# Kernel tuning notes

Hardware: AMD Instinct MI355X
Metric: run time of the kernel (lower is better)

Reference implementation:

```python
import jax, jax.numpy as jnp
import numpy as np

EMBED_DIM = 1024


def setup_inputs() -> dict:
    key = jax.random.key(0)
    ks = jax.random.split(key, 9)
    d = EMBED_DIM
    s = 1.0 / np.sqrt(d)
    x = jax.random.normal(ks[0], (4, 2048, d), dtype=jnp.float32)
    # nn.Linear weights are [out, in]; we store them transposed for x @ W
    Wq = jax.random.uniform(ks[1], (d, d), jnp.float32, -s, s)
    bq = jax.random.uniform(ks[2], (d,), jnp.float32, -s, s)
    Wk = jax.random.uniform(ks[3], (d, d), jnp.float32, -s, s)
    bk = jax.random.uniform(ks[4], (d,), jnp.float32, -s, s)
    Wv = jax.random.uniform(ks[5], (d, d), jnp.float32, -s, s)
    bv = jax.random.uniform(ks[6], (d,), jnp.float32, -s, s)
    Wo = jax.random.uniform(ks[7], (d, d), jnp.float32, -s, s)
    bo = jax.random.uniform(ks[8], (d,), jnp.float32, -s, s)
    return {"x": x, "Wq": Wq, "bq": bq, "Wk": Wk, "bk": bk,
            "Wv": Wv, "bv": bv, "Wo": Wo, "bo": bo}


def reference(x, Wq, bq, Wk, bk, Wv, bv, Wo, bo):
    b, seq_len, d = x.shape
    scaling = 1.0 / jnp.sqrt(jnp.float32(d))
    q = x @ Wq + bq  # [b, s, d]
    k = x @ Wk + bk
    v = x @ Wv + bv
    scores = jnp.einsum('bqd,bkd->bqk', q, k) * scaling  # [b, s, s]
    causal = jnp.tril(jnp.ones((seq_len, seq_len), dtype=bool))
    scores = jnp.where(causal, scores, -jnp.inf)
    attn = jax.nn.softmax(scores, axis=-1)
    out = jnp.einsum('bqk,bkd->bqd', attn, v)
    return out @ Wo + bo
```

## Files before the change

kernel.cpp:

```cpp
#include <hip/hip_runtime.h>
#include <stdint.h>

typedef __bf16 bf16_t;
typedef __bf16 bf16x8 __attribute__((ext_vector_type(8)));
typedef __bf16 bf16x4 __attribute__((ext_vector_type(4)));
typedef float  f32x4  __attribute__((ext_vector_type(4)));

#define DEV __device__ __forceinline__

constexpr int S = 2048, D = 1024, BATCH = 4, MF = BATCH * S;

DEV void gload16(const void* g, void* l) {
  __builtin_amdgcn_global_load_lds(
      (const __attribute__((address_space(1))) void*)g,
      (__attribute__((address_space(3))) void*)(uint32_t)(uintptr_t)l,
      16, 0, 0);
}

template<int EP>
DEV void gemm_body(int tm, int tn, int bz,
                   const bf16_t* __restrict__ A, const bf16_t* __restrict__ B,
                   void* __restrict__ C0, void* __restrict__ C1,
                   void* __restrict__ C2, const float* __restrict__ aux,
                   int K, int kmax, bf16_t* ldsA, bf16_t* ldsB)
{
  const int m0 = tm * 128, n0 = tn * 128;
  const int tid  = threadIdx.x;
  const int lane = tid & 63;
  const int wave = tid >> 6;
  const int wm = wave & 1, wn = wave >> 1;
  const int l8r = lane >> 3;
  const int swz = ((lane & 7) ^ (lane >> 3)) * 8;
  const int cl  = lane & 15;
  const int qd  = lane >> 4;
  const int ch0 = ((qd ^ (cl & 7)) * 8);

  f32x4 acc[4][4] = {};

  for (int k0 = 0; k0 < kmax; k0 += 64) {
    #pragma unroll
    for (int t = 0; t < 4; ++t) {
      const int rb = wave * 4 + t;
      gload16(A + (long)(m0 + rb * 8 + l8r) * K + (k0 + swz), &ldsA[rb * 512]);
      gload16(B + (long)(n0 + rb * 8 + l8r) * K + (k0 + swz), &ldsB[rb * 512]);
    }
    __syncthreads();
    #pragma unroll
    for (int kk = 0; kk < 64; kk += 32) {
      bf16x8 af[4], bg[4];
      #pragma unroll
      for (int i = 0; i < 4; ++i)
        af[i] = *(const bf16x8*)&ldsA[(wm * 64 + i * 16 + cl) * 64 + (ch0 ^ kk)];
      #pragma unroll
      for (int j = 0; j < 4; ++j)
        bg[j] = *(const bf16x8*)&ldsB[(wn * 64 + j * 16 + cl) * 64 + (ch0 ^ kk)];
      #pragma unroll
      for (int i = 0; i < 4; ++i)
        #pragma unroll
        for (int j = 0; j < 4; ++j)
          acc[i][j] = __builtin_amdgcn_mfma_f32_16x16x32_bf16(af[i], bg[j], acc[i][j], 0, 0, 0);
    }
    __syncthreads();
  }

  #pragma unroll
  for (int i = 0; i < 4; ++i) {
    const int gm0 = m0 + wm * 64 + i * 16 + qd * 4;

    if (EP == 1) {
      uint8_t* q8 = (uint8_t*)C0;
      uint8_t* k8 = (uint8_t*)C1;
      bf16_t* vwT = (bf16_t*)C2;
      #pragma unroll
      for (int j = 0; j < 4; ++j) {
        const int gn  = n0 + wn * 64 + j * 16 + cl;
        const int sec = gn >> 10, ln = gn & 1023;
        const float bn = aux[gn];
        if (sec == 2) {
          const int z = gm0 >> 11, s0 = gm0 & 2047;
          bf16x4 v4;
          #pragma unroll
          for (int r = 0; r < 4; ++r) v4[r] = (bf16_t)(acc[i][j][r] + bn);
          *(bf16x4*)&vwT[((long)z * D + ln) * S + s0] = v4;
        } else {
          uint8_t* dst = (sec == 0) ? q8 : k8;
          #pragma unroll
          for (int r = 0; r < 4; ++r) {
            const float v = acc[i][j][r] + bn;
            const int p = __builtin_amdgcn_cvt_pk_fp8_f32(v, v, 0, false);
            dst[(long)(gm0 + r) * D + ln] = (uint8_t)(p & 0xFF);
          }
        }
      }
    }

    if (EP == 3) {
      float* out = (float*)C0 + (long)bz * S * D;
      const float* invl = aux + (long)bz * S;
      const float* bo = (const float*)C1;
      float scl[4];
      #pragma unroll
      for (int r = 0; r < 4; ++r) scl[r] = invl[gm0 + r];
      #pragma unroll
      for (int j = 0; j < 4; ++j) {
        const int gn = n0 + wn * 64 + j * 16 + cl;
        const float bn = bo[gn];
        #pragma unroll
        for (int r = 0; r < 4; ++r)
          out[(long)(gm0 + r) * D + gn] = acc[i][j][r] * scl[r] + bn;
      }
    }

    if (EP == 4) {
      bf16_t* Co = (bf16_t*)C0;
      #pragma unroll
      for (int j = 0; j < 4; ++j) {
        const int gn = n0 + wn * 64 + j * 16 + cl;
        #pragma unroll
        for (int r = 0; r < 4; ++r)
          Co[(long)(gm0 + r) * D + gn] = (bf16_t)acc[i][j][r];
      }
    }
  }
}

__global__ __launch_bounds__(256, 4) void gemm_qkv(
    const bf16_t* __restrict__ A, const bf16_t* __restrict__ B,
    uint8_t* q8, uint8_t* k8, bf16_t* vwT, const float* __restrict__ bias)
{
  __shared__ __align__(16) bf16_t lA[128 * 64], lB[128 * 64];
  gemm_body<1>(blockIdx.x, blockIdx.y, 0, A, B, q8, k8, vwT, bias,
               1024, 1024, lA, lB);
}

__global__ __launch_bounds__(256, 4) void gemm_sc8(
    const uint8_t* __restrict__ q8g, const uint8_t* __restrict__ k8g,
    bf16_t* __restrict__ probs_g, float* __restrict__ part)
{
  __shared__ __align__(16) uint8_t lA[128 * 64], lB[128 * 64];
  const int l = blockIdx.x, xcd = l & 7, idx = l >> 3;
  const int bz = xcd >> 1;
  const int t  = (xcd & 1) * 68 + idx;
  int tm = (int)((sqrtf(8.0f * t + 1.0f) - 1.0f) * 0.5f);
  while ((tm + 1) * (tm + 2) / 2 <= t) ++tm;
  while (tm * (tm + 1) / 2 > t) --tm;
  const int tn = t - tm * (tm + 1) / 2;
  const int m0 = tm * 128, n0 = tn * 128;
  const uint8_t* q8 = q8g + (long)bz * S * D;
  const uint8_t* k8 = k8g + (long)bz * S * D;

  const int tid  = threadIdx.x;
  const int lane = tid & 63;
  const int wave = tid >> 6;
  const int wm = wave & 1, wn = wave >> 1;
  const int srow = lane >> 2;
  const int sgr  = (lane & 3) ^ ((lane >> 3) & 3);
  const int cl = lane & 15, qd = lane >> 4;
  const int sfr = (cl >> 1) & 3;
  const int half8 = (qd & 1) * 8;

  f32x4 acc[4][4] = {};

  for (int k0 = 0; k0 < 1024; k0 += 64) {
    #pragma unroll
    for (int tt = 0; tt < 2; ++tt) {
      const int rb = wave * 2 + tt;
      const int gr = rb * 16 + srow;
      gload16(q8 + (long)(m0 + gr) * 1024 + k0 + sgr * 16, &lA[rb * 1024]);
      gload16(k8 + (long)(n0 + gr) * 1024 + k0 + sgr * 16, &lB[rb * 1024]);
    }
    __syncthreads();
    #pragma unroll
    for (int kk = 0; kk < 2; ++kk) {
      long a[4], b[4];
      const int pg = ((kk << 1) + (qd >> 1)) ^ sfr;
      #pragma unroll
      for (int i = 0; i < 4; ++i)
        a[i] = *(const long*)&lA[(wm * 64 + i * 16 + cl) * 64 + pg * 16 + half8];
      #pragma unroll
      for (int j = 0; j < 4; ++j)
        b[j] = *(const long*)&lB[(wn * 64 + j * 16 + cl) * 64 + pg * 16 + half8];
      #pragma unroll
      for (int i = 0; i < 4; ++i)
        #pragma unroll
        for (int j = 0; j < 4; ++j)
          acc[i][j] = __builtin_amdgcn_mfma_f32_16x16x32_fp8_fp8(a[i], b[j], acc[i][j], 0, 0, 0);
    }
    __syncthreads();
  }

  bf16_t* probs = probs_g + (long)bz * S * S;
  #pragma unroll
  for (int i = 0; i < 4; ++i) {
    const int gm0 = m0 + wm * 64 + i * 16 + qd * 4;
    float ls[4] = {0.f, 0.f, 0.f, 0.f};
    #pragma unroll
    for (int j = 0; j < 4; ++j) {
      const int gn = n0 + wn * 64 + j * 16 + cl;
      #pragma unroll
      for (int r = 0; r < 4; ++r) {
        const int gm = gm0 + r;
        const float e = (gn <= gm) ? __expf(acc[i][j][r] * 0.03125f) : 0.0f;
        probs[(long)gm * S + gn] = (bf16_t)e;
        ls[r] += e;
      }
    }
    #pragma unroll
    for (int r = 0; r < 4; ++r) {
      float v = ls[r];
      v += __shfl_xor(v, 1); v += __shfl_xor(v, 2);
      v += __shfl_xor(v, 4); v += __shfl_xor(v, 8);
      if (cl == 0)
        part[((long)bz * S + (gm0 + r)) * 32 + tn * 2 + wn] = v;
    }
  }
}

__global__ __launch_bounds__(256, 4) void gemm_pv_out(
    const bf16_t* __restrict__ probs, const bf16_t* __restrict__ vwT,
    float* out, const float* __restrict__ invl, const float* __restrict__ bo)
{
  __shared__ __align__(16) bf16_t lA[128 * 64], lB[128 * 64];
  const int l = blockIdx.x, xcd = l & 7, idx = l >> 3;
  const int bz = xcd >> 1, half = xcd & 1;
  const int g = (idx >> 3) & 3, tn = idx & 7;
  const int tm = (idx < 32) ? (15 - half - 2 * g) : (2 * g + half);
  const int kmax = (tm + 1) * 128;
  gemm_body<3>(tm, tn, bz, probs + (long)bz * S * S, vwT + (long)bz * D * S,
               out, (void*)bo, nullptr, invl, 2048, kmax, lA, lB);
}

__global__ __launch_bounds__(256, 4) void gemm_wvo(
    const bf16_t* __restrict__ WoT, const bf16_t* __restrict__ WvN,
    bf16_t* WvoT)
{
  __shared__ __align__(16) bf16_t lA[128 * 64], lB[128 * 64];
  gemm_body<4>(blockIdx.x, blockIdx.y, 0, WoT, WvN, WvoT, nullptr, nullptr,
               nullptr, 1024, 1024, lA, lB);
}

__global__ __launch_bounds__(256) void reduce_invl(
    const float* __restrict__ part, float* __restrict__ invl)
{
  const int r = blockIdx.x * 256 + threadIdx.x;
  const int row = r & (S - 1);
  const int cnt = ((row >> 7) + 1) * 2;
  const float* p = part + (long)r * 32;
  float s = 0.f;
  for (int j = 0; j < cnt; ++j) s += p[j];
  invl[r] = 1.0f / s;
}

__global__ __launch_bounds__(256) void cvt_x(
    const float4* __restrict__ in, bf16x4* __restrict__ out, int n4)
{
  const int i = blockIdx.x * 256 + threadIdx.x;
  if (i >= n4) return;
  float4 f = in[i];
  bf16x4 o;
  o.x = (__bf16)f.x; o.y = (__bf16)f.y; o.z = (__bf16)f.z; o.w = (__bf16)f.w;
  out[i] = o;
}

__global__ __launch_bounds__(256) void cvt_w_t4(
    const float* __restrict__ W0, const float* __restrict__ W1,
    const float* __restrict__ W2, const float* __restrict__ W3,
    bf16_t* __restrict__ dst)
{
  const int zmap[4] = {0, 1, 3, 4};
  const float* W = (blockIdx.z == 0) ? W0 : (blockIdx.z == 1) ? W1
                 : (blockIdx.z == 2) ? W2 : W3;
  bf16_t* WT = dst + (size_t)zmap[blockIdx.z] * D * D;
  const int bx = blockIdx.x, by = blockIdx.y;
  const int tx = threadIdx.x & 31, ty = threadIdx.x >> 5;

  if (blockIdx.z == 2) {
    #pragma unroll
    for (int dy = 0; dy < 32; dy += 8) {
      const long idx = (long)(by * 32 + ty + dy) * 1024 + bx * 32 + tx;
      WT[idx] = (bf16_t)W[idx];
    }
    return;
  }

  __shared__ float t[32][33];
  #pragma unroll
  for (int dy = 0; dy < 32; dy += 8)
    t[ty + dy][tx] = W[(long)(by * 32 + ty + dy) * 1024 + bx * 32 + tx];
  __syncthreads();
  #pragma unroll
  for (int dy = 0; dy < 32; dy += 8)
    WT[(long)(bx * 32 + ty + dy) * 1024 + by * 32 + tx] = (bf16_t)t[tx][ty + dy];
}

__global__ __launch_bounds__(256) void bias_build(
    const float* __restrict__ bq, const float* __restrict__ bk,
    const float* __restrict__ bv, const bf16_t* __restrict__ WoT,
    float* __restrict__ o)
{
  const int b = blockIdx.x;
  if (b >= 256) {
    const int i = (b - 256) * 256 + threadIdx.x;
    o[i] = bq[i];
    o[1024 + i] = bk[i];
    return;
  }
  const int wave = threadIdx.x >> 6, lane = threadIdx.x & 63;
  const int c = b * 4 + wave;
  const bf16_t* row = WoT + (long)c * 1024 + lane * 16;
  const float*  bvp = bv + lane * 16;
  float s = 0.f;
  #pragma unroll
  for (int j = 0; j < 16; ++j) s += bvp[j] * (float)row[j];
  #pragma unroll
  for (int sh = 32; sh > 0; sh >>= 1) s += __shfl_xor(s, sh, 64);
  if (lane == 0) o[2048 + c] = s;
}

extern "C" void kernel_launch(void* const* d_in, const int* in_sizes, int n_in,
                              void* d_out, int out_size, void* d_ws, size_t ws_size,
                              hipStream_t stream) {
  const float* x  = (const float*)d_in[0];
  const float* Wq = (const float*)d_in[1];
  const float* bq = (const float*)d_in[2];
  const float* Wk = (const float*)d_in[3];
  const float* bk = (const float*)d_in[4];
  const float* Wv = (const float*)d_in[5];
  const float* bv = (const float*)d_in[6];
  const float* Wo = (const float*)d_in[7];
  const float* bo = (const float*)d_in[8];
  float* out = (float*)d_out;

  size_t off = 0;
  auto alloc = [&](size_t bytes) -> void* {
    void* p = (char*)d_ws + off;
    off += (bytes + 255) & ~(size_t)255;
    return p;
  };
  bf16_t* x_b   = (bf16_t*)alloc((size_t)MF * D * 2);
  bf16_t* Wall  = (bf16_t*)alloc((size_t)5 * D * D * 2);
  float*  bqkv  = (float*) alloc((size_t)3 * D * 4);
  uint8_t* q8   = (uint8_t*)alloc((size_t)MF * D);
  uint8_t* k8   = (uint8_t*)alloc((size_t)MF * D);
  bf16_t* vwT_b = (bf16_t*)alloc((size_t)BATCH * D * S * 2);
  bf16_t* probs = (bf16_t*)alloc((size_t)BATCH * S * S * 2);
  float*  part  = (float*) alloc((size_t)MF * 32 * 4);
  float*  invl  = (float*) alloc((size_t)MF * 4);
  bf16_t* WqkvT = Wall;
  bf16_t* WvoT  = Wall + (size_t)2 * D * D;
  bf16_t* WvN   = Wall + (size_t)3 * D * D;
  bf16_t* WoT   = Wall + (size_t)4 * D * D;

  cvt_x<<<dim3((MF * D / 4 + 255) / 256), 256, 0, stream>>>(
      (const float4*)x, (bf16x4*)x_b, MF * D / 4);
  cvt_w_t4<<<dim3(32, 32, 4), 256, 0, stream>>>(Wq, Wk, Wv, Wo, Wall);
  bias_build<<<dim3(260), 256, 0, stream>>>(bq, bk, bv, WoT, bqkv);

  gemm_wvo<<<dim3(8, 8), 256, 0, stream>>>(WoT, WvN, WvoT);

  gemm_qkv<<<dim3(64, 24), 256, 0, stream>>>(x_b, WqkvT, q8, k8, vwT_b, bqkv);

  gemm_sc8<<<dim3(544), 256, 0, stream>>>(q8, k8, probs, part);

  reduce_invl<<<dim3(MF / 256), 256, 0, stream>>>(part, invl);

  gemm_pv_out<<<dim3(512), 256, 0, stream>>>(probs, vwT_b, out, invl, bo);
}
```

Before: 249.1 us.

## Replace QKV GEMM with 256x256-tile, 8-wave, double-buffered pipelined kernel

Replaces the 128x128-tile QKV projection GEMM with a dedicated 256x256-tile kernel using 512 threads, a double-buffered LDS pipeline of async global-to-LDS loads, and four interleaved MFMA quarter-phases separated by explicit barriers and setprio hints. Larger tiles raise arithmetic intensity and cut global traffic per FLOP. Overlapping the next K-slice loads with compute is meant to hide memory latency. In exchange it uses 128KB of LDS and many accumulator registers, which limits occupancy. The grid shrinks to 384 blocks, which may leave the 256 CUs unevenly loaded.

```diff
diff --git a/kernel.cpp b/kernel.cpp
--- a/kernel.cpp
+++ b/kernel.cpp
@@ -16,6 +16,9 @@
       (__attribute__((address_space(3))) void*)(uint32_t)(uintptr_t)l,
       16, 0, 0);
 }
+
+#define BAR() asm volatile("s_barrier" ::: "memory")
+#define WAIT_LGKM0() asm volatile("s_waitcnt lgkmcnt(0)" ::: "memory")
 
 template<int EP>
 DEV void gemm_body(int tm, int tn, int bz,
@@ -67,33 +70,6 @@
   for (int i = 0; i < 4; ++i) {
     const int gm0 = m0 + wm * 64 + i * 16 + qd * 4;
 
-    if (EP == 1) {
-      uint8_t* q8 = (uint8_t*)C0;
-      uint8_t* k8 = (uint8_t*)C1;
-      bf16_t* vwT = (bf16_t*)C2;
-      #pragma unroll
-      for (int j = 0; j < 4; ++j) {
-        const int gn  = n0 + wn * 64 + j * 16 + cl;
-        const int sec = gn >> 10, ln = gn & 1023;
-        const float bn = aux[gn];
-        if (sec == 2) {
-          const int z = gm0 >> 11, s0 = gm0 & 2047;
-          bf16x4 v4;
-          #pragma unroll
-          for (int r = 0; r < 4; ++r) v4[r] = (bf16_t)(acc[i][j][r] + bn);
-          *(bf16x4*)&vwT[((long)z * D + ln) * S + s0] = v4;
-        } else {
-          uint8_t* dst = (sec == 0) ? q8 : k8;
-          #pragma unroll
-          for (int r = 0; r < 4; ++r) {
-            const float v = acc[i][j][r] + bn;
-            const int p = __builtin_amdgcn_cvt_pk_fp8_f32(v, v, 0, false);
-            dst[(long)(gm0 + r) * D + ln] = (uint8_t)(p & 0xFF);
-          }
-        }
-      }
-    }
-
     if (EP == 3) {
       float* out = (float*)C0 + (long)bz * S * D;
       const float* invl = aux + (long)bz * S;
@@ -124,13 +100,153 @@
   }
 }
 
-__global__ __launch_bounds__(256, 4) void gemm_qkv(
+DEV void stA256(const bf16_t* A, int m0, int k0, bf16_t* dst,
+                int qh, int wave, int l8r, int swz) {
+  #pragma unroll
+  for (int t = 0; t < 2; ++t) {
+    const int ib = wave * 2 + t;
+    const int rb = ((ib >> 3) << 7) | (qh << 6) | ((ib & 7) << 3);
+    gload16(A + (long)(m0 + rb + l8r) * 1024 + (k0 + swz), dst + rb * 64);
+  }
+}
+
+DEV void stB256(const bf16_t* B, int n0, int k0, bf16_t* dst,
+                int qh, int wave, int l8r, int swz) {
+  #pragma unroll
+  for (int t = 0; t < 2; ++t) {
+    const int ib = wave * 2 + t;
+    const int rb = ((ib >> 2) << 6) | (qh << 5) | ((ib & 3) << 3);
+    gload16(B + (long)(n0 + rb + l8r) * 1024 + (k0 + swz), dst + rb * 64);
+  }
+}
+
+DEV void readA4(bf16x8 (&a)[4][2], const bf16_t* base, int row0, int cl, int ch0) {
+  #pragma unroll
+  for (int i = 0; i < 4; ++i) {
+    const bf16_t* p = base + (row0 + i * 16 + cl) * 64;
+    a[i][0] = *(const bf16x8*)(p + ch0);
+    a[i][1] = *(const bf16x8*)(p + (ch0 ^ 32));
+  }
+}
+
+DEV void readB2(bf16x8 (&b)[2][2], const bf16_t* base, int row0, int cl, int ch0) {
+  #pragma unroll
+  for (int jj = 0; jj < 2; ++jj) {
+    const bf16_t* p = base + (row0 + jj * 16 + cl) * 64;
+    b[jj][0] = *(const bf16x8*)(p + ch0);
+    b[jj][1] = *(const bf16x8*)(p + (ch0 ^ 32));
+  }
+}
+
+template<int MH, int NH>
+DEV void qphase(f32x4 (&acc)[8][4], const bf16x8 (&a)[4][2], const bf16x8 (&b)[2][2]) {
+  __builtin_amdgcn_s_setprio(1);
+  #pragma unroll
+  for (int i = 0; i < 4; ++i)
+    #pragma unroll
+    for (int jj = 0; jj < 2; ++jj)
+      #pragma unroll
+      for (int kk = 0; kk < 2; ++kk)
+        acc[MH * 4 + i][NH * 2 + jj] = __builtin_amdgcn_mfma_f32_16x16x32_bf16(
+            a[i][kk], b[jj][kk], acc[MH * 4 + i][NH * 2 + jj], 0, 0, 0);
+  __builtin_amdgcn_s_setprio(0);
+}
+
+__global__ __launch_bounds__(512, 2) void gemm_qkv256(
     const bf16_t* __restrict__ A, const bf16_t* __restrict__ B,
-    uint8_t* q8, uint8_t* k8, bf16_t* vwT, const float* __restrict__ bias)
-{
-  __shared__ __align__(16) bf16_t lA[128 * 64], lB[128 * 64];
-  gemm_body<1>(blockIdx.x, blockIdx.y, 0, A, B, q8, k8, vwT, bias,
-               1024, 1024, lA, lB);
+    uint8_t* __restrict__ q8, uint8_t* __restrict__ k8,
+    bf16_t* __restrict__ vwT, const float* __restrict__ aux)
+{
+  __shared__ __align__(16) bf16_t lA[2][256 * 64], lB[2][256 * 64];
+  const int m0 = blockIdx.x * 256, n0 = blockIdx.y * 256;
+  const int tid = threadIdx.x, lane = tid & 63, wave = tid >> 6;
+  const int wm = wave & 1, wn = wave >> 1;
+  const int l8r = lane >> 3, swz = ((lane & 7) ^ l8r) * 8;
+  const int cl = lane & 15, qd = lane >> 4;
+  const int ch0 = (qd ^ (cl & 7)) * 8;
+
+  f32x4 acc[8][4] = {};
+  bf16x8 a[4][2], b0[2][2], b1[2][2];
+
+  stA256(A, m0,  0, lA[0], 0, wave, l8r, swz);
+  stB256(B, n0,  0, lB[0], 0, wave, l8r, swz);
+  stB256(B, n0,  0, lB[0], 1, wave, l8r, swz);
+  stA256(A, m0,  0, lA[0], 1, wave, l8r, swz);
+  stA256(A, m0, 64, lA[1], 0, wave, l8r, swz);
+  stB256(B, n0, 64, lB[1], 0, wave, l8r, swz);
+  stB256(B, n0, 64, lB[1], 1, wave, l8r, swz);
+  asm volatile("s_waitcnt vmcnt(6)" ::: "memory");
+  BAR();
+
+  for (int t = 0; t < 16; ++t) {
+    const int cur = t & 1;
+    const bf16_t* cA = lA[cur];
+    const bf16_t* cB = lB[cur];
+    bf16_t* nAbuf = lA[cur ^ 1];
+    bf16_t* cAbuf = lA[cur];
+    bf16_t* cBbuf = lB[cur];
+    const int rA = wm * 128, rB = wn * 64;
+    const int kn1 = (t + 1) * 64, kn2 = (t + 2) * 64;
+
+    readA4(a, cA, rA, cl, ch0);
+    readB2(b0, cB, rB, cl, ch0);
+    if (t < 15) stA256(A, m0, kn1, nAbuf, 1, wave, l8r, swz);
+    BAR();
+    WAIT_LGKM0();
+    qphase<0, 0>(acc, a, b0);
+    BAR();
+
+    readB2(b1, cB, rB + 32, cl, ch0);
+    if (t < 14) stA256(A, m0, kn2, cAbuf, 0, wave, l8r, swz);
+    BAR();
+    WAIT_LGKM0();
+    qphase<0, 1>(acc, a, b1);
+    BAR();
+
+    readA4(a, cA, rA + 64, cl, ch0);
+    if (t < 14) stB256(B, n0, kn2, cBbuf, 0, wave, l8r, swz);
+    BAR();
+    WAIT_LGKM0();
+    qphase<1, 0>(acc, a, b0);
+    BAR();
+
+    if (t < 14) {
+      stB256(B, n0, kn2, cBbuf, 1, wave, l8r, swz);
+      asm volatile("s_waitcnt vmcnt(6)" ::: "memory");
+    } else if (t == 14) {
+      asm volatile("s_waitcnt vmcnt(0)" ::: "memory");
+    }
+    BAR();
+    WAIT_LGKM0();
+    qphase<1, 1>(acc, a, b1);
+    BAR();
+  }
+
+  #pragma unroll
+  for (int ai = 0; ai < 8; ++ai) {
+    const int gm0 = m0 + wm * 128 + ai * 16 + qd * 4;
+    #pragma unroll
+    for (int aj = 0; aj < 4; ++aj) {
+      const int gn  = n0 + wn * 64 + aj * 16 + cl;
+      const int sec = gn >> 10, ln = gn & 1023;
+      const float bn = aux[gn];
+      if (sec == 2) {
+        const int z = gm0 >> 11, s0 = gm0 & 2047;
+        bf16x4 v4;
+        #pragma unroll
+        for (int r = 0; r < 4; ++r) v4[r] = (bf16_t)(acc[ai][aj][r] + bn);
+        *(bf16x4*)&vwT[((long)z * D + ln) * S + s0] = v4;
+      } else {
+        uint8_t* dst = (sec == 0) ? q8 : k8;
+        #pragma unroll
+        for (int r = 0; r < 4; ++r) {
+          const float v = acc[ai][aj][r] + bn;
+          const int p = __builtin_amdgcn_cvt_pk_fp8_f32(v, v, 0, false);
+          dst[(long)(gm0 + r) * D + ln] = (uint8_t)(p & 0xFF);
+        }
+      }
+    }
+  }
 }
 
 __global__ __launch_bounds__(256, 4) void gemm_sc8(
@@ -358,7 +474,7 @@
 
   gemm_wvo<<<dim3(8, 8), 256, 0, stream>>>(WoT, WvN, WvoT);
 
-  gemm_qkv<<<dim3(64, 24), 256, 0, stream>>>(x_b, WqkvT, q8, k8, vwT_b, bqkv);
+  gemm_qkv256<<<dim3(32, 12), 512, 0, stream>>>(x_b, WqkvT, q8, k8, vwT_b, bqkv);
 
   gemm_sc8<<<dim3(544), 256, 0, stream>>>(q8, k8, probs, part);
 
```

Result: slower. 259.2 us (+4.1%).

## Use 64x128 score tiles and fold row-sum reduction into PV kernel

Applied to the files above, without the earlier changes.

The QK^T fp8 score kernel now uses 64-row by 128-column tiles, giving 1088 blocks over the causal triangle instead of 544 128x128 tiles. This trims wasted work on diagonal tiles and improves load balance, and the occupancy hint is raised to 6. The separate reduce_invl kernel is removed: the PV/output kernel now sums the per-row partial sums into shared memory before its GEMM, which saves a launch and an intermediate buffer. In exchange, the smaller tiles mean less data reuse per loaded byte, and every PV block redundantly re-reads the partials.

```diff
diff --git a/kernel.cpp b/kernel.cpp
--- a/kernel.cpp
+++ b/kernel.cpp
@@ -94,13 +94,13 @@
       }
     }
 
-    if (EP == 3) {
+    if (EP == 5) {
       float* out = (float*)C0 + (long)bz * S * D;
-      const float* invl = aux + (long)bz * S;
       const float* bo = (const float*)C1;
+      const float* invl_l = aux;
       float scl[4];
       #pragma unroll
-      for (int r = 0; r < 4; ++r) scl[r] = invl[gm0 + r];
+      for (int r = 0; r < 4; ++r) scl[r] = invl_l[wm * 64 + i * 16 + qd * 4 + r];
       #pragma unroll
       for (int j = 0; j < 4; ++j) {
         const int gn = n0 + wn * 64 + j * 16 + cl;
@@ -133,58 +133,60 @@
                1024, 1024, lA, lB);
 }
 
-__global__ __launch_bounds__(256, 4) void gemm_sc8(
+__global__ __launch_bounds__(256, 6) void gemm_sc8(
     const uint8_t* __restrict__ q8g, const uint8_t* __restrict__ k8g,
     bf16_t* __restrict__ probs_g, float* __restrict__ part)
 {
-  __shared__ __align__(16) uint8_t lA[128 * 64], lB[128 * 64];
+  __shared__ __align__(16) uint8_t lA[64 * 64], lB[128 * 64];
   const int l = blockIdx.x, xcd = l & 7, idx = l >> 3;
   const int bz = xcd >> 1;
-  const int t  = (xcd & 1) * 68 + idx;
-  int tm = (int)((sqrtf(8.0f * t + 1.0f) - 1.0f) * 0.5f);
-  while ((tm + 1) * (tm + 2) / 2 <= t) ++tm;
-  while (tm * (tm + 1) / 2 > t) --tm;
-  const int tn = t - tm * (tm + 1) / 2;
-  const int m0 = tm * 128, n0 = tn * 128;
+  const int t  = (xcd & 1) * 136 + idx;
+  int a0 = (int)((sqrtf(4.0f * t + 1.0f) - 1.0f) * 0.5f);
+  while ((a0 + 1) * (a0 + 2) <= t) ++a0;
+  while (a0 * (a0 + 1) > t) --a0;
+  int r64, tn;
+  if (t >= (a0 + 1) * (a0 + 1)) { r64 = 2 * a0 + 1; tn = t - (a0 + 1) * (a0 + 1); }
+  else                          { r64 = 2 * a0;     tn = t - a0 * (a0 + 1); }
+  const int m0 = r64 * 64, n0 = tn * 128;
   const uint8_t* q8 = q8g + (long)bz * S * D;
   const uint8_t* k8 = k8g + (long)bz * S * D;
 
   const int tid  = threadIdx.x;
   const int lane = tid & 63;
-  const int wave = tid >> 6;
-  const int wm = wave & 1, wn = wave >> 1;
+  const int wn   = tid >> 6;
   const int srow = lane >> 2;
   const int sgr  = (lane & 3) ^ ((lane >> 3) & 3);
   const int cl = lane & 15, qd = lane >> 4;
   const int sfr = (cl >> 1) & 3;
   const int half8 = (qd & 1) * 8;
 
-  f32x4 acc[4][4] = {};
+  f32x4 acc[4][2] = {};
 
   for (int k0 = 0; k0 < 1024; k0 += 64) {
+    gload16(q8 + (long)(m0 + wn * 16 + srow) * 1024 + k0 + sgr * 16,
+            &lA[wn * 1024]);
     #pragma unroll
     for (int tt = 0; tt < 2; ++tt) {
-      const int rb = wave * 2 + tt;
-      const int gr = rb * 16 + srow;
-      gload16(q8 + (long)(m0 + gr) * 1024 + k0 + sgr * 16, &lA[rb * 1024]);
-      gload16(k8 + (long)(n0 + gr) * 1024 + k0 + sgr * 16, &lB[rb * 1024]);
+      const int rb = wn * 2 + tt;
+      gload16(k8 + (long)(n0 + rb * 16 + srow) * 1024 + k0 + sgr * 16,
+              &lB[rb * 1024]);
     }
     __syncthreads();
     #pragma unroll
     for (int kk = 0; kk < 2; ++kk) {
-      long a[4], b[4];
+      long av[4], bv[2];
       const int pg = ((kk << 1) + (qd >> 1)) ^ sfr;
       #pragma unroll
       for (int i = 0; i < 4; ++i)
-        a[i] = *(const long*)&lA[(wm * 64 + i * 16 + cl) * 64 + pg * 16 + half8];
-      #pragma unroll
-      for (int j = 0; j < 4; ++j)
-        b[j] = *(const long*)&lB[(wn * 64 + j * 16 + cl) * 64 + pg * 16 + half8];
+        av[i] = *(const long*)&lA[(i * 16 + cl) * 64 + pg * 16 + half8];
+      #pragma unroll
+      for (int j = 0; j < 2; ++j)
+        bv[j] = *(const long*)&lB[(wn * 32 + j * 16 + cl) * 64 + pg * 16 + half8];
       #pragma unroll
       for (int i = 0; i < 4; ++i)
         #pragma unroll
-        for (int j = 0; j < 4; ++j)
-          acc[i][j] = __builtin_amdgcn_mfma_f32_16x16x32_fp8_fp8(a[i], b[j], acc[i][j], 0, 0, 0);
+        for (int j = 0; j < 2; ++j)
+          acc[i][j] = __builtin_amdgcn_mfma_f32_16x16x32_fp8_fp8(av[i], bv[j], acc[i][j], 0, 0, 0);
     }
     __syncthreads();
   }
@@ -192,11 +194,11 @@
   bf16_t* probs = probs_g + (long)bz * S * S;
   #pragma unroll
   for (int i = 0; i < 4; ++i) {
-    const int gm0 = m0 + wm * 64 + i * 16 + qd * 4;
+    const int gm0 = m0 + i * 16 + qd * 4;
     float ls[4] = {0.f, 0.f, 0.f, 0.f};
     #pragma unroll
-    for (int j = 0; j < 4; ++j) {
-      const int gn = n0 + wn * 64 + j * 16 + cl;
+    for (int j = 0; j < 2; ++j) {
+      const int gn = n0 + wn * 32 + j * 16 + cl;
       #pragma unroll
       for (int r = 0; r < 4; ++r) {
         const int gm = gm0 + r;
@@ -211,23 +213,35 @@
       v += __shfl_xor(v, 1); v += __shfl_xor(v, 2);
       v += __shfl_xor(v, 4); v += __shfl_xor(v, 8);
       if (cl == 0)
-        part[((long)bz * S + (gm0 + r)) * 32 + tn * 2 + wn] = v;
+        part[((long)bz * S + (gm0 + r)) * 64 + tn * 4 + wn] = v;
     }
   }
 }
 
 __global__ __launch_bounds__(256, 4) void gemm_pv_out(
     const bf16_t* __restrict__ probs, const bf16_t* __restrict__ vwT,
-    float* out, const float* __restrict__ invl, const float* __restrict__ bo)
+    float* out, const float* __restrict__ part, const float* __restrict__ bo)
 {
   __shared__ __align__(16) bf16_t lA[128 * 64], lB[128 * 64];
+  __shared__ float invl_s[128];
   const int l = blockIdx.x, xcd = l & 7, idx = l >> 3;
   const int bz = xcd >> 1, half = xcd & 1;
   const int g = (idx >> 3) & 3, tn = idx & 7;
   const int tm = (idx < 32) ? (15 - half - 2 * g) : (2 * g + half);
   const int kmax = (tm + 1) * 128;
-  gemm_body<3>(tm, tn, bz, probs + (long)bz * S * S, vwT + (long)bz * D * S,
-               out, (void*)bo, nullptr, invl, 2048, kmax, lA, lB);
+
+  if (threadIdx.x < 128) {
+    const int row = tm * 128 + threadIdx.x;
+    const int cnt = (tm + 1) * 4;
+    const float* p = part + ((long)bz * S + row) * 64;
+    float s = 0.f;
+    for (int j = 0; j < cnt; ++j) s += p[j];
+    invl_s[threadIdx.x] = 1.0f / s;
+  }
+  __syncthreads();
+
+  gemm_body<5>(tm, tn, bz, probs + (long)bz * S * S, vwT + (long)bz * D * S,
+               out, (void*)bo, nullptr, invl_s, 2048, kmax, lA, lB);
 }
 
 __global__ __launch_bounds__(256, 4) void gemm_wvo(
@@ -237,18 +251,6 @@
   __shared__ __align__(16) bf16_t lA[128 * 64], lB[128 * 64];
   gemm_body<4>(blockIdx.x, blockIdx.y, 0, WoT, WvN, WvoT, nullptr, nullptr,
                nullptr, 1024, 1024, lA, lB);
-}
-
-__global__ __launch_bounds__(256) void reduce_invl(
-    const float* __restrict__ part, float* __restrict__ invl)
-{
-  const int r = blockIdx.x * 256 + threadIdx.x;
-  const int row = r & (S - 1);
-  const int cnt = ((row >> 7) + 1) * 2;
-  const float* p = part + (long)r * 32;
-  float s = 0.f;
-  for (int j = 0; j < cnt; ++j) s += p[j];
-  invl[r] = 1.0f / s;
 }
 
 __global__ __launch_bounds__(256) void cvt_x(
@@ -344,8 +346,7 @@
   uint8_t* k8   = (uint8_t*)alloc((size_t)MF * D);
   bf16_t* vwT_b = (bf16_t*)alloc((size_t)BATCH * D * S * 2);
   bf16_t* probs = (bf16_t*)alloc((size_t)BATCH * S * S * 2);
-  float*  part  = (float*) alloc((size_t)MF * 32 * 4);
-  float*  invl  = (float*) alloc((size_t)MF * 4);
+  float*  part  = (float*) alloc((size_t)MF * 64 * 4);
   bf16_t* WqkvT = Wall;
   bf16_t* WvoT  = Wall + (size_t)2 * D * D;
   bf16_t* WvN   = Wall + (size_t)3 * D * D;
@@ -360,9 +361,7 @@
 
   gemm_qkv<<<dim3(64, 24), 256, 0, stream>>>(x_b, WqkvT, q8, k8, vwT_b, bqkv);
 
-  gemm_sc8<<<dim3(544), 256, 0, stream>>>(q8, k8, probs, part);
-
-  reduce_invl<<<dim3(MF / 256), 256, 0, stream>>>(part, invl);
-
-  gemm_pv_out<<<dim3(512), 256, 0, stream>>>(probs, vwT_b, out, invl, bo);
-}
+  gemm_sc8<<<dim3(1088), 256, 0, stream>>>(q8, k8, probs, part);
+
+  gemm_pv_out<<<dim3(512), 256, 0, stream>>>(probs, vwT_b, out, part, bo);
+}
```

New measurement: 250.6 us. Within noise of the previous version (+0.6%).

## Deepen K-step per barrier and fuse softmax row-sum reduction into PV GEMM

Applied to the files above, without the earlier changes.

The GEMM loops for the score and PV kernels now stage two 64-wide K slices per barrier pair, which halves synchronisation count per K and gives more loads in flight, at the cost of doubled LDS usage. The PV kernel's occupancy hint drops to 2. The separate reduce_invl kernel is removed and each PV block computes its 128 row inverse-sums from the partials into shared memory before the GEMM, saving a launch and a global round trip at the cost of redundant reduction across the 8 column tiles.

```diff
diff --git a/kernel.cpp b/kernel.cpp
--- a/kernel.cpp
+++ b/kernel.cpp
@@ -17,7 +17,7 @@
       16, 0, 0);
 }
 
-template<int EP>
+template<int EP, int NSUB>
 DEV void gemm_body(int tm, int tn, int bz,
                    const bf16_t* __restrict__ A, const bf16_t* __restrict__ B,
                    void* __restrict__ C0, void* __restrict__ C1,
@@ -37,28 +37,36 @@
 
   f32x4 acc[4][4] = {};
 
-  for (int k0 = 0; k0 < kmax; k0 += 64) {
-    #pragma unroll
-    for (int t = 0; t < 4; ++t) {
-      const int rb = wave * 4 + t;
-      gload16(A + (long)(m0 + rb * 8 + l8r) * K + (k0 + swz), &ldsA[rb * 512]);
-      gload16(B + (long)(n0 + rb * 8 + l8r) * K + (k0 + swz), &ldsB[rb * 512]);
+  for (int k0 = 0; k0 < kmax; k0 += 64 * NSUB) {
+    #pragma unroll
+    for (int h = 0; h < NSUB; ++h) {
+      #pragma unroll
+      for (int t = 0; t < 4; ++t) {
+        const int rb = wave * 4 + t;
+        gload16(A + (long)(m0 + rb * 8 + l8r) * K + (k0 + h * 64 + swz),
+                &ldsA[h * 8192 + rb * 512]);
+        gload16(B + (long)(n0 + rb * 8 + l8r) * K + (k0 + h * 64 + swz),
+                &ldsB[h * 8192 + rb * 512]);
+      }
     }
     __syncthreads();
     #pragma unroll
-    for (int kk = 0; kk < 64; kk += 32) {
-      bf16x8 af[4], bg[4];
-      #pragma unroll
-      for (int i = 0; i < 4; ++i)
-        af[i] = *(const bf16x8*)&ldsA[(wm * 64 + i * 16 + cl) * 64 + (ch0 ^ kk)];
-      #pragma unroll
-      for (int j = 0; j < 4; ++j)
-        bg[j] = *(const bf16x8*)&ldsB[(wn * 64 + j * 16 + cl) * 64 + (ch0 ^ kk)];
-      #pragma unroll
-      for (int i = 0; i < 4; ++i)
+    for (int h = 0; h < NSUB; ++h) {
+      #pragma unroll
+      for (int kk = 0; kk < 64; kk += 32) {
+        bf16x8 af[4], bg[4];
+        #pragma unroll
+        for (int i = 0; i < 4; ++i)
+          af[i] = *(const bf16x8*)&ldsA[h * 8192 + (wm * 64 + i * 16 + cl) * 64 + (ch0 ^ kk)];
         #pragma unroll
         for (int j = 0; j < 4; ++j)
-          acc[i][j] = __builtin_amdgcn_mfma_f32_16x16x32_bf16(af[i], bg[j], acc[i][j], 0, 0, 0);
+          bg[j] = *(const bf16x8*)&ldsB[h * 8192 + (wn * 64 + j * 16 + cl) * 64 + (ch0 ^ kk)];
+        #pragma unroll
+        for (int i = 0; i < 4; ++i)
+          #pragma unroll
+          for (int j = 0; j < 4; ++j)
+            acc[i][j] = __builtin_amdgcn_mfma_f32_16x16x32_bf16(af[i], bg[j], acc[i][j], 0, 0, 0);
+      }
     }
     __syncthreads();
   }
@@ -94,13 +102,13 @@
       }
     }
 
-    if (EP == 3) {
+    if (EP == 5) {
       float* out = (float*)C0 + (long)bz * S * D;
-      const float* invl = aux + (long)bz * S;
       const float* bo = (const float*)C1;
+      const float* invl_l = aux;
       float scl[4];
       #pragma unroll
-      for (int r = 0; r < 4; ++r) scl[r] = invl[gm0 + r];
+      for (int r = 0; r < 4; ++r) scl[r] = invl_l[wm * 64 + i * 16 + qd * 4 + r];
       #pragma unroll
       for (int j = 0; j < 4; ++j) {
         const int gn = n0 + wn * 64 + j * 16 + cl;
@@ -129,15 +137,15 @@
     uint8_t* q8, uint8_t* k8, bf16_t* vwT, const float* __restrict__ bias)
 {
   __shared__ __align__(16) bf16_t lA[128 * 64], lB[128 * 64];
-  gemm_body<1>(blockIdx.x, blockIdx.y, 0, A, B, q8, k8, vwT, bias,
-               1024, 1024, lA, lB);
+  gemm_body<1, 1>(blockIdx.x, blockIdx.y, 0, A, B, q8, k8, vwT, bias,
+                  1024, 1024, lA, lB);
 }
 
 __global__ __launch_bounds__(256, 4) void gemm_sc8(
     const uint8_t* __restrict__ q8g, const uint8_t* __restrict__ k8g,
     bf16_t* __restrict__ probs_g, float* __restrict__ part)
 {
-  __shared__ __align__(16) uint8_t lA[128 * 64], lB[128 * 64];
+  __shared__ __align__(16) uint8_t lA[2][128 * 64], lB[2][128 * 64];
   const int l = blockIdx.x, xcd = l & 7, idx = l >> 3;
   const int bz = xcd >> 1;
   const int t  = (xcd & 1) * 68 + idx;
@@ -161,30 +169,38 @@
 
   f32x4 acc[4][4] = {};
 
-  for (int k0 = 0; k0 < 1024; k0 += 64) {
-    #pragma unroll
-    for (int tt = 0; tt < 2; ++tt) {
-      const int rb = wave * 2 + tt;
-      const int gr = rb * 16 + srow;
-      gload16(q8 + (long)(m0 + gr) * 1024 + k0 + sgr * 16, &lA[rb * 1024]);
-      gload16(k8 + (long)(n0 + gr) * 1024 + k0 + sgr * 16, &lB[rb * 1024]);
+  for (int k0 = 0; k0 < 1024; k0 += 128) {
+    #pragma unroll
+    for (int h = 0; h < 2; ++h) {
+      #pragma unroll
+      for (int tt = 0; tt < 2; ++tt) {
+        const int rb = wave * 2 + tt;
+        const int gr = rb * 16 + srow;
+        gload16(q8 + (long)(m0 + gr) * 1024 + k0 + h * 64 + sgr * 16,
+                &lA[h][rb * 1024]);
+        gload16(k8 + (long)(n0 + gr) * 1024 + k0 + h * 64 + sgr * 16,
+                &lB[h][rb * 1024]);
+      }
     }
     __syncthreads();
     #pragma unroll
-    for (int kk = 0; kk < 2; ++kk) {
-      long a[4], b[4];
-      const int pg = ((kk << 1) + (qd >> 1)) ^ sfr;
-      #pragma unroll
-      for (int i = 0; i < 4; ++i)
-        a[i] = *(const long*)&lA[(wm * 64 + i * 16 + cl) * 64 + pg * 16 + half8];
-      #pragma unroll
-      for (int j = 0; j < 4; ++j)
-        b[j] = *(const long*)&lB[(wn * 64 + j * 16 + cl) * 64 + pg * 16 + half8];
-      #pragma unroll
-      for (int i = 0; i < 4; ++i)
+    for (int h = 0; h < 2; ++h) {
+      #pragma unroll
+      for (int kk = 0; kk < 2; ++kk) {
+        long a[4], b[4];
+        const int pg = ((kk << 1) + (qd >> 1)) ^ sfr;
+        #pragma unroll
+        for (int i = 0; i < 4; ++i)
+          a[i] = *(const long*)&lA[h][(wm * 64 + i * 16 + cl) * 64 + pg * 16 + half8];
         #pragma unroll
         for (int j = 0; j < 4; ++j)
-          acc[i][j] = __builtin_amdgcn_mfma_f32_16x16x32_fp8_fp8(a[i], b[j], acc[i][j], 0, 0, 0);
+          b[j] = *(const long*)&lB[h][(wn * 64 + j * 16 + cl) * 64 + pg * 16 + half8];
+        #pragma unroll
+        for (int i = 0; i < 4; ++i)
+          #pragma unroll
+          for (int j = 0; j < 4; ++j)
+            acc[i][j] = __builtin_amdgcn_mfma_f32_16x16x32_fp8_fp8(a[i], b[j], acc[i][j], 0, 0, 0);
+      }
     }
     __syncthreads();
   }
@@ -216,18 +232,30 @@
   }
 }
 
-__global__ __launch_bounds__(256, 4) void gemm_pv_out(
+__global__ __launch_bounds__(256, 2) void gemm_pv_out(
     const bf16_t* __restrict__ probs, const bf16_t* __restrict__ vwT,
-    float* out, const float* __restrict__ invl, const float* __restrict__ bo)
-{
-  __shared__ __align__(16) bf16_t lA[128 * 64], lB[128 * 64];
+    float* out, const float* __restrict__ part, const float* __restrict__ bo)
+{
+  __shared__ __align__(16) bf16_t lA[2 * 128 * 64], lB[2 * 128 * 64];
+  __shared__ float invl_s[128];
   const int l = blockIdx.x, xcd = l & 7, idx = l >> 3;
   const int bz = xcd >> 1, half = xcd & 1;
   const int g = (idx >> 3) & 3, tn = idx & 7;
   const int tm = (idx < 32) ? (15 - half - 2 * g) : (2 * g + half);
   const int kmax = (tm + 1) * 128;
-  gemm_body<3>(tm, tn, bz, probs + (long)bz * S * S, vwT + (long)bz * D * S,
-               out, (void*)bo, nullptr, invl, 2048, kmax, lA, lB);
+
+  if (threadIdx.x < 128) {
+    const int row = tm * 128 + threadIdx.x;
+    const int cnt = (tm + 1) * 2;
+    const float* p = part + ((long)bz * S + row) * 32;
+    float s = 0.f;
+    for (int j = 0; j < cnt; ++j) s += p[j];
+    invl_s[threadIdx.x] = 1.0f / s;
+  }
+  __syncthreads();
+
+  gemm_body<5, 2>(tm, tn, bz, probs + (long)bz * S * S, vwT + (long)bz * D * S,
+                  out, (void*)bo, nullptr, invl_s, 2048, kmax, lA, lB);
 }
 
 __global__ __launch_bounds__(256, 4) void gemm_wvo(
@@ -235,20 +263,8 @@
     bf16_t* WvoT)
 {
   __shared__ __align__(16) bf16_t lA[128 * 64], lB[128 * 64];
-  gemm_body<4>(blockIdx.x, blockIdx.y, 0, WoT, WvN, WvoT, nullptr, nullptr,
-               nullptr, 1024, 1024, lA, lB);
-}
-
-__global__ __launch_bounds__(256) void reduce_invl(
-    const float* __restrict__ part, float* __restrict__ invl)
-{
-  const int r = blockIdx.x * 256 + threadIdx.x;
-  const int row = r & (S - 1);
-  const int cnt = ((row >> 7) + 1) * 2;
-  const float* p = part + (long)r * 32;
-  float s = 0.f;
-  for (int j = 0; j < cnt; ++j) s += p[j];
-  invl[r] = 1.0f / s;
+  gemm_body<4, 1>(blockIdx.x, blockIdx.y, 0, WoT, WvN, WvoT, nullptr, nullptr,
+                  nullptr, 1024, 1024, lA, lB);
 }
 
 __global__ __launch_bounds__(256) void cvt_x(
@@ -345,7 +361,6 @@
   bf16_t* vwT_b = (bf16_t*)alloc((size_t)BATCH * D * S * 2);
   bf16_t* probs = (bf16_t*)alloc((size_t)BATCH * S * S * 2);
   float*  part  = (float*) alloc((size_t)MF * 32 * 4);
-  float*  invl  = (float*) alloc((size_t)MF * 4);
   bf16_t* WqkvT = Wall;
   bf16_t* WvoT  = Wall + (size_t)2 * D * D;
   bf16_t* WvN   = Wall + (size_t)3 * D * D;
@@ -362,7 +377,5 @@
 
   gemm_sc8<<<dim3(544), 256, 0, stream>>>(q8, k8, probs, part);
 
-  reduce_invl<<<dim3(MF / 256), 256, 0, stream>>>(part, invl);
-
-  gemm_pv_out<<<dim3(512), 256, 0, stream>>>(probs, vwT_b, out, invl, bo);
-}
+  gemm_pv_out<<<dim3(512), 256, 0, stream>>>(probs, vwT_b, out, part, bo);
+}
```

Result: faster. 243.5 us (-2.3%).
